# Kernel tuning notes

Hardware: AMD Instinct MI355X
Metric: run time of the kernel (lower is better)

The kernel has to match this reference:

```python
import jax, jax.numpy as jnp
import numpy as np

B0, C0, H0, W0 = 2, 64, 48, 48
BR, DI, NS, RK, K = 128, 128, 16, 4, 4
EPS = 1e-5


def _bn_relu(x, g, b):
    # eval-mode BatchNorm2d (running mean 0, var 1) followed by ReLU; x is NCHW
    return jax.nn.relu(x * (g / jnp.sqrt(1.0 + EPS))[None, :, None, None] + b[None, :, None, None])


def _c1(x, w):
    # 1x1 conv, w: (O, C, 1, 1)
    return jnp.einsum('bchw,oc->bohw', x, w[:, :, 0, 0])


def _avgpool(x, k, s, p):
    # torch AvgPool2d with count_include_pad=True -> divide by k*k
    y = jax.lax.reduce_window(x, 0.0, jax.lax.add, (1, 1, k, k), (1, 1, s, s), ((0, 0), (0, 0), (p, p), (p, p)))
    return y / float(k * k)


def _resize(x, h, w):
    # bilinear, align_corners=False (half-pixel), NCHW
    return jax.image.resize(x, (x.shape[0], x.shape[1], h, w), 'bilinear')


def _pappm(x, s0_g, s0_b, s0_w, s1_g, s1_b, s1_w, s2_g, s2_b, s2_w, s3_g, s3_b, s3_w, s4_g, s4_b, s4_w, comp_g, comp_b, comp_w, sc_g, sc_b, sc_w):
    h, w = x.shape[2], x.shape[3]
    x0 = _c1(_bn_relu(x, s0_g, s0_b), s0_w)
    y1 = _c1(_bn_relu(_avgpool(x, 3, 1, 1), s1_g, s1_b), s1_w) + x0  # stride-1 pool keeps size
    y2 = _resize(_c1(_bn_relu(_avgpool(x, 5, 2, 2), s2_g, s2_b), s2_w), h, w) + x0
    y3 = _resize(_c1(_bn_relu(_avgpool(x, 9, 4, 4), s3_g, s3_b), s3_w), h, w) + x0
    y4 = _c1(_bn_relu(x.mean((2, 3), keepdims=True), s4_g, s4_b), s4_w) + x0  # 1x1 -> broadcast
    cat = jnp.concatenate([x0, y1, y2, y3, y4], axis=1)  # (B, 5*BR, H, W)
    comp = jax.lax.conv_general_dilated(_bn_relu(cat, comp_g, comp_b), comp_w, (1, 1), ((1, 1), (1, 1)), dimension_numbers=('NCHW', 'OIHW', 'NCHW'))
    return comp + _c1(_bn_relu(x, sc_g, sc_b), sc_w)


def _ss2d(xin, in_proj_w, dw_w, dw_b, x_proj_w, dt_w, dt_b, A_logs, Ds, ln_g, ln_b, out_proj_w):
    # xin: (B, H, W, d_model)
    Bb, Hh, Ww, _ = xin.shape
    xz = xin @ in_proj_w.T                      # (B,H,W,2*DI)
    xc, z = jnp.split(xz, 2, axis=-1)
    xc = jnp.transpose(xc, (0, 3, 1, 2))        # (B,DI,H,W)
    xc = jax.lax.conv_general_dilated(xc, dw_w, (1, 1), ((1, 1), (1, 1)), dimension_numbers=('NCHW', 'OIHW', 'NCHW'), feature_group_count=DI)
    xc = jax.nn.silu(xc + dw_b[None, :, None, None])
    L = Hh * Ww
    x_hw = xc.reshape(Bb, DI, L)
    x_wh = jnp.transpose(xc, (0, 1, 3, 2)).reshape(Bb, DI, L)
    xs = jnp.stack([x_hw, x_wh, x_hw[:, :, ::-1], x_wh[:, :, ::-1]], axis=1)  # (B,K,DI,L)
    x_dbl = jnp.einsum('bkdl,kcd->bkcl', xs, x_proj_w)
    dts, Bm, Cm = jnp.split(x_dbl, [RK, RK + NS], axis=2)  # (B,K,RK,L),(B,K,NS,L),(B,K,NS,L)
    delta = jax.nn.softplus(jnp.einsum('bkrl,kdr->bkdl', dts, dt_w) + dt_b[None, :, :, None])  # (B,K,DI,L)
    A = -jnp.exp(A_logs).reshape(K, DI, NS)
    a = jnp.exp(delta[..., None] * A[None, :, :, None, :])                    # (B,K,DI,L,NS)
    bu = (delta * xs)[..., None] * jnp.transpose(Bm, (0, 1, 3, 2))[:, :, None]  # (B,K,DI,L,NS)

    def comb(e1, e2):
        a1, b1 = e1
        a2, b2 = e2
        return a2 * a1, a2 * b1 + b2

    _, hst = jax.lax.associative_scan(comb, (a, bu), axis=3)  # h_t = a_t*h_{t-1} + b_t
    y = jnp.einsum('bkdln,bknl->bkdl', hst, Cm) + xs * Ds.reshape(K, DI)[None, :, :, None]
    inv = y[:, 2:4][:, :, :, ::-1]
    y3 = jnp.transpose(y[:, 1].reshape(Bb, DI, Ww, Hh), (0, 1, 3, 2)).reshape(Bb, DI, L)
    y4 = jnp.transpose(inv[:, 1].reshape(Bb, DI, Ww, Hh), (0, 1, 3, 2)).reshape(Bb, DI, L)
    ys = jnp.transpose(y[:, 0] + inv[:, 0] + y3 + y4, (0, 2, 1)).reshape(Bb, Hh, Ww, DI)
    mu = ys.mean(-1, keepdims=True)
    var = jnp.mean((ys - mu) ** 2, -1, keepdims=True)
    yn = (ys - mu) / jnp.sqrt(var + EPS) * ln_g + ln_b
    return (yn * jax.nn.silu(z)) @ out_proj_w.T  # (B,H,W,d_model)


def setup_inputs():
    key = jax.random.key(0)
    ks = iter(jax.random.split(key, 32))
    nrm = lambda shp, s: jax.random.normal(next(ks), shp, jnp.float32) * s
    d = {}
    d['x'] = nrm((B0, C0, H0, W0), 1.0)
    for nm in ['s0', 's1', 's2', 's3', 's4']:
        d[nm + '_g'] = jnp.ones((C0,), jnp.float32)
        d[nm + '_b'] = jnp.zeros((C0,), jnp.float32)
        d[nm + '_w'] = nrm((BR, C0, 1, 1), (2.0 / C0) ** 0.5)
    d['comp_g'] = jnp.ones((5 * BR,), jnp.float32)
    d['comp_b'] = jnp.zeros((5 * BR,), jnp.float32)
    d['comp_w'] = nrm((C0, 5 * BR, 3, 3), (2.0 / (5 * BR * 9)) ** 0.5)
    d['sc_g'] = jnp.ones((C0,), jnp.float32)
    d['sc_b'] = jnp.zeros((C0,), jnp.float32)
    d['sc_w'] = nrm((C0, C0, 1, 1), (2.0 / C0) ** 0.5)
    d['in_proj_w'] = nrm((2 * DI, C0), C0 ** -0.5)
    d['dw_w'] = nrm((DI, 1, 3, 3), 0.3)
    d['dw_b'] = jnp.zeros((DI,), jnp.float32)
    d['x_proj_w'] = nrm((K, RK + 2 * NS, DI), DI ** -0.5)
    d['dt_w'] = nrm((K, DI, RK), RK ** -0.5)
    d['dt_b'] = jnp.log(jnp.expm1(jnp.asarray(0.01, jnp.float32))) * jnp.ones((K, DI), jnp.float32)
    d['A_logs'] = jnp.tile(jnp.log(jnp.arange(1, NS + 1, dtype=jnp.float32))[None], (K * DI, 1))
    d['Ds'] = jnp.ones((K * DI,), jnp.float32)
    d['ln_g'] = jnp.ones((DI,), jnp.float32)
    d['ln_b'] = jnp.zeros((DI,), jnp.float32)
    d['out_proj_w'] = nrm((C0, DI), DI ** -0.5)
    d['fc1_w'] = nrm((BR, C0, 1, 1), C0 ** -0.5)
    d['fc1_b'] = jnp.zeros((BR,), jnp.float32)
    d['fc2_w'] = nrm((C0, BR, 1, 1), BR ** -0.5)
    d['fc2_b'] = jnp.zeros((C0,), jnp.float32)
    return d


def reference(x, s0_g, s0_b, s0_w, s1_g, s1_b, s1_w, s2_g, s2_b, s2_w, s3_g, s3_b, s3_w, s4_g, s4_b, s4_w, comp_g, comp_b, comp_w, sc_g, sc_b, sc_w, in_proj_w, dw_w, dw_b, x_proj_w, dt_w, dt_b, A_logs, Ds, ln_g, ln_b, out_proj_w, fc1_w, fc1_b, fc2_w, fc2_b):
    p = _pappm(x, s0_g, s0_b, s0_w, s1_g, s1_b, s1_w, s2_g, s2_b, s2_w, s3_g, s3_b, s3_w, s4_g, s4_b, s4_w, comp_g, comp_b, comp_w, sc_g, sc_b, sc_w)
    a = _ss2d(jnp.transpose(p, (0, 2, 3, 1)), in_proj_w, dw_w, dw_b, x_proj_w, dt_w, dt_b, A_logs, Ds, ln_g, ln_b, out_proj_w)
    x1 = jnp.transpose(a, (0, 3, 1, 2))  # (B,C0,H,W)
    h1 = jax.nn.silu(_c1(x1, fc1_w) + fc1_b[None, :, None, None])
    return _c1(h1, fc2_w) + fc2_b[None, :, None, None] + x1
```

## Files before the change

### kernel.cpp

```cpp
#include <hip/hip_runtime.h>
#include <math.h>

constexpr int cB = 2, cC = 64, cH = 48, cW = 48, cL = 48 * 48;
constexpr int cBR = 128, cDI = 128, cNS = 16, cRK = 4, cK = 4;
constexpr float cEPS = 1e-5f;
constexpr int NCH = 32;
constexpr int CHL = cL / NCH;
constexpr int KTOT = 5824;

typedef unsigned short u16;
typedef unsigned int u32;
typedef short s16x8 __attribute__((ext_vector_type(8)));
typedef float f32x4 __attribute__((ext_vector_type(4)));

__device__ __forceinline__ float bnrelu(float v, float g, float b) {
    float y = v * (g * rsqrtf(1.0f + cEPS)) + b;
    return y > 0.f ? y : 0.f;
}
__device__ __forceinline__ float silu(float v) {
    return v / (1.f + expf(-v));
}
__device__ __forceinline__ u16 f2bf(float f) {
    u32 u = __float_as_uint(f);
    u = (u + 0x7fffu + ((u >> 16) & 1u)) >> 16;
    return (u16)u;
}
__device__ __forceinline__ s16x8 cvt8(const float* p) {
    s16x8 r;
#pragma unroll
    for (int i = 0; i < 8; i++) r[i] = (short)f2bf(p[i]);
    return r;
}
__device__ __forceinline__ float row_sum16(float v) {
    v += __int_as_float(__builtin_amdgcn_update_dpp(0, __float_as_int(v), 0xB1, 0xF, 0xF, true));
    v += __int_as_float(__builtin_amdgcn_update_dpp(0, __float_as_int(v), 0x4E, 0xF, 0xF, true));
    v += __int_as_float(__builtin_amdgcn_update_dpp(0, __float_as_int(v), 0x124, 0xF, 0xF, true));
    v += __int_as_float(__builtin_amdgcn_update_dpp(0, __float_as_int(v), 0x128, 0xF, 0xF, true));
    return v;
}

__global__ void __launch_bounds__(256) k_pools(const float* __restrict__ x, float* __restrict__ pool3,
                                               float* __restrict__ pool5, float* __restrict__ pool9,
                                               float* __restrict__ gmean) {
    __shared__ float sm[4];
    int blk = blockIdx.x;
    int t = threadIdx.x;
    if (blk < 1152) {
        int idx = blk * 256 + t;
        int w = idx % cW, h = (idx / cW) % cH, bc = idx / cL;
        const float* p = x + bc * cL;
        float s = 0.f;
        for (int dh = -1; dh <= 1; dh++) {
            int hh = h + dh; if (hh < 0 || hh >= cH) continue;
            for (int dw = -1; dw <= 1; dw++) {
                int ww = w + dw; if (ww < 0 || ww >= cW) continue;
                s += p[hh * cW + ww];
            }
        }
        pool3[idx] = s * (1.f / 9.f);
    } else if (blk < 1440) {
        int idx = (blk - 1152) * 256 + t;
        int w = idx % 24, h = (idx / 24) % 24, bc = idx / 576;
        const float* p = x + bc * cL;
        float s = 0.f;
        for (int kh = 0; kh < 5; kh++) {
            int hh = h * 2 - 2 + kh; if (hh < 0 || hh >= cH) continue;
            for (int kw = 0; kw < 5; kw++) {
                int ww = w * 2 - 2 + kw; if (ww < 0 || ww >= cW) continue;
                s += p[hh * cW + ww];
            }
        }
        pool5[idx] = s * (1.f / 25.f);
    } else if (blk < 1512) {
        int idx = (blk - 1440) * 256 + t;
        int w = idx % 12, h = (idx / 12) % 12, bc = idx / 144;
        const float* p = x + bc * cL;
        float s = 0.f;
        for (int kh = 0; kh < 9; kh++) {
            int hh = h * 4 - 4 + kh; if (hh < 0 || hh >= cH) continue;
            for (int kw = 0; kw < 9; kw++) {
                int ww = w * 4 - 4 + kw; if (ww < 0 || ww >= cW) continue;
                s += p[hh * cW + ww];
            }
        }
        pool9[idx] = s * (1.f / 81.f);
    } else {
        int bc = blk - 1512;
        const float* p = x + bc * cL;
        float s = 0.f;
        for (int i = t; i < cL; i += 256) s += p[i];
        for (int m = 32; m > 0; m >>= 1) s += __shfl_down(s, m);
        if ((t & 63) == 0) sm[t >> 6] = s;
        __syncthreads();
        if (t == 0) gmean[bc] = (sm[0] + sm[1] + sm[2] + sm[3]) * (1.f / cL);
    }
}

__global__ void __launch_bounds__(256) k_prep(const float* __restrict__ cw, const float* __restrict__ scw,
                                              const float* __restrict__ s0w, const float* __restrict__ s1w,
                                              const float* __restrict__ ipw, const float* __restrict__ xpw,
                                              u16* __restrict__ w8, u16* __restrict__ wcat,
                                              u16* __restrict__ ipk, u16* __restrict__ xpk) {
    int blk = blockIdx.x, t = threadIdx.x;
    if (blk < 1456) {
        int idx = blk * 256 + t;
        int o = idx / KTOT, kx = idx % KTOT;
        float v;
        if (kx < 5760) { int tap = kx / 640, ch = kx % 640; v = cw[(o * 640 + ch) * 9 + tap]; }
        else v = scw[o * 64 + (kx - 5760)];
        w8[(((size_t)(kx >> 3) * 64) + o) * 8 + (kx & 7)] = f2bf(v);
    } else if (blk < 1520) {
        int idx = (blk - 1456) * 256 + t;
        int g = idx >> 13, r = idx & 8191;
        int o = r >> 6, c = r & 63;
        float v = (g ? s1w : s0w)[r];
        int kt = c >> 5, q = (c >> 3) & 3, j = c & 7, nt = o >> 4, ln = o & 15;
        wcat[(size_t)((((g * 2 + kt) * 4 + q) * 8 + nt) * 16 + ln) * 8 + j] = f2bf(v);
    } else if (blk < 1584) {
        int idx = (blk - 1520) * 256 + t;
        int o = idx >> 6, c = idx & 63;
        int kt = c >> 5, q = (c >> 3) & 3, j = c & 7, nt = o >> 4, ln = o & 15;
        ipk[(size_t)(((kt * 4 + q) * 16 + nt) * 16 + ln) * 8 + j] = f2bf(ipw[idx]);
    } else {
        int idx = (blk - 1584) * 256 + t;
        int o = idx >> 7, d = idx & 127;
        int kt = d >> 5, q = (d >> 3) & 3, j = d & 7, nt = o >> 4, ln = o & 15;
        xpk[(size_t)(((kt * 4 + q) * 9 + nt) * 16 + ln) * 8 + j] = f2bf(xpw[idx]);
    }
}

__global__ void __launch_bounds__(128) k_c1all(const float* __restrict__ pool5, const float* __restrict__ pool9,
                                               const float* __restrict__ gm,
                                               const float* __restrict__ s2g, const float* __restrict__ s2b,
                                               const float* __restrict__ s2w,
                                               const float* __restrict__ s3g, const float* __restrict__ s3b,
                                               const float* __restrict__ s3w,
                                               const float* __restrict__ s4g, const float* __restrict__ s4b,
                                               const float* __restrict__ s4w,
                                               float* __restrict__ c2cl, float* __restrict__ c3cl,
                                               float* __restrict__ c4) {
    int pos = blockIdx.x;
    const float *in, *g, *bb, *w;
    float* outp;
    int HW, b, pp;
    if (pos < cB * 576) { b = pos / 576; pp = pos % 576; in = pool5; g = s2g; bb = s2b; w = s2w; HW = 576; outp = c2cl + ((size_t)b * 576 + pp) * 128; }
    else if (pos < cB * 576 + cB * 144) { int r = pos - cB * 576; b = r / 144; pp = r % 144; in = pool9; g = s3g; bb = s3b; w = s3w; HW = 144; outp = c3cl + ((size_t)b * 144 + pp) * 128; }
    else { b = pos - cB * 576 - cB * 144; pp = 0; in = gm; g = s4g; bb = s4b; w = s4w; HW = 1; outp = c4 + (size_t)b * 128; }
    __shared__ float v[64];
    int t = threadIdx.x;
    if (t < 64) v[t] = bnrelu(in[(b * 64 + t) * HW + pp], g[t], bb[t]);
    __syncthreads();
    float acc = 0.f;
    const float* wr = w + t * 64;
#pragma unroll 16
    for (int c = 0; c < 64; c++) acc += v[c] * wr[c];
    outp[t] = acc;
}

__global__ void __launch_bounds__(256) k_cat2(
    const float* __restrict__ x, const float* __restrict__ pool3, const float* __restrict__ c4,
    const float* __restrict__ s0g, const float* __restrict__ s0b,
    const float* __restrict__ s1g, const float* __restrict__ s1b,
    const float* __restrict__ scg, const float* __restrict__ scb,
    const float* __restrict__ cg, const float* __restrict__ cbb,
    const u16* __restrict__ wcat, const float* __restrict__ c2cl, const float* __restrict__ c3cl,
    u16* __restrict__ catbf, u16* __restrict__ xbf) {
    int blk = blockIdx.x;
    int b = blk / 144;
    int l0 = (blk % 144) * 16;
    int t = threadIdx.x;
    __shared__ float axv[16][68];
    __shared__ float ap3[16][68];
    __shared__ u16 axc[16][66];
    int pc = t >> 4, p = t & 15;
#pragma unroll
    for (int i = 0; i < 4; i++) {
        int c = i * 16 + pc;
        float xraw = x[(size_t)(b * 64 + c) * cL + l0 + p];
        float p3raw = pool3[(size_t)(b * 64 + c) * cL + l0 + p];
        axv[p][c] = bnrelu(xraw, s0g[c], s0b[c]);
        ap3[p][c] = bnrelu(p3raw, s1g[c], s1b[c]);
        axc[p][c] = f2bf(bnrelu(xraw, scg[c], scb[c]));
    }
    __syncthreads();
#pragma unroll
    for (int i = 0; i < 4; i++) {
        int idx = i * 256 + t;
        int pp = idx >> 6, cc = idx & 63;
        xbf[((size_t)b * cL + l0 + pp) * 64 + cc] = axc[pp][cc];
    }
    int wv = t >> 6, lane = t & 63, ln = lane & 15, q = lane >> 4;
    f32x4 ax[2] = {};
    f32x4 ay[2] = {};
#pragma unroll
    for (int kt = 0; kt < 2; kt++) {
        s16x8 a0 = cvt8(&axv[ln][kt * 32 + q * 8]);
        s16x8 a1 = cvt8(&ap3[ln][kt * 32 + q * 8]);
#pragma unroll
        for (int jj = 0; jj < 2; jj++) {
            int nt = wv * 2 + jj;
            s16x8 b0 = *(const s16x8*)(wcat + (size_t)((((0 * 2 + kt) * 4 + q) * 8 + nt) * 16 + ln) * 8);
            s16x8 b1 = *(const s16x8*)(wcat + (size_t)((((1 * 2 + kt) * 4 + q) * 8 + nt) * 16 + ln) * 8);
            ax[jj] = __builtin_amdgcn_mfma_f32_16x16x32_bf16(a0, b0, ax[jj], 0, 0, 0);
            ay[jj] = __builtin_amdgcn_mfma_f32_16x16x32_bf16(a1, b1, ay[jj], 0, 0, 0);
        }
    }
    int hrow = l0 / cW, w0g = l0 % cW;
    float sy2 = hrow * 0.5f - 0.25f;
    float fy2 = floorf(sy2); int iy2 = (int)fy2; float ay2 = sy2 - fy2;
    int y20 = min(max(iy2, 0), 23), y21 = min(max(iy2 + 1, 0), 23);
    float sy3 = hrow * 0.25f - 0.375f;
    float fy3 = floorf(sy3); int iy3 = (int)fy3; float ay3 = sy3 - fy3;
    int y30 = min(max(iy3, 0), 11), y31 = min(max(iy3 + 1, 0), 11);
    const float* c2b = c2cl + (size_t)b * 576 * 128;
    const float* c3b = c3cl + (size_t)b * 144 * 128;
#pragma unroll
    for (int r = 0; r < 4; r++) {
        int pp = q * 4 + r;
        int wq = w0g + pp;
        float sx2 = wq * 0.5f - 0.25f;
        float fx2 = floorf(sx2); int ix2 = (int)fx2; float ax2 = sx2 - fx2;
        int x20 = min(max(ix2, 0), 23), x21 = min(max(ix2 + 1, 0), 23);
        float sx3 = wq * 0.25f - 0.375f;
        float fx3 = floorf(sx3); int ix3 = (int)fx3; float ax3 = sx3 - fx3;
        int x30 = min(max(ix3, 0), 11), x31 = min(max(ix3 + 1, 0), 11);
#pragma unroll
        for (int jj = 0; jj < 2; jj++) {
            int ch = (wv * 2 + jj) * 16 + ln;
            float v00 = c2b[(y20 * 24 + x20) * 128 + ch], v01 = c2b[(y20 * 24 + x21) * 128 + ch];
            float v10 = c2b[(y21 * 24 + x20) * 128 + ch], v11 = c2b[(y21 * 24 + x21) * 128 + ch];
            float t0 = v00 + (v01 - v00) * ax2, t1 = v10 + (v11 - v10) * ax2;
            float u2v = t0 + (t1 - t0) * ay2;
            float w00 = c3b[(y30 * 12 + x30) * 128 + ch], w01 = c3b[(y30 * 12 + x31) * 128 + ch];
            float w10 = c3b[(y31 * 12 + x30) * 128 + ch], w11 = c3b[(y31 * 12 + x31) * 128 + ch];
            float s0_ = w00 + (w01 - w00) * ax3, s1_ = w10 + (w11 - w10) * ax3;
            float u3v = s0_ + (s1_ - s0_) * ay3;
            float x0 = ax[jj][r];
            float y1 = ay[jj][r] + x0;
            float y2 = x0 + u2v;
            float y3 = x0 + u3v;
            float y4 = x0 + c4[b * 128 + ch];
            u16* base = catbf + ((size_t)b * cL + l0 + pp) * 640;
            base[ch]       = f2bf(bnrelu(x0, cg[ch],       cbb[ch]));
            base[128 + ch] = f2bf(bnrelu(y1, cg[128 + ch], cbb[128 + ch]));
            base[256 + ch] = f2bf(bnrelu(y2, cg[256 + ch], cbb[256 + ch]));
            base[384 + ch] = f2bf(bnrelu(y3, cg[384 + ch], cbb[384 + ch]));
            base[512 + ch] = f2bf(bnrelu(y4, cg[512 + ch], cbb[512 + ch]));
        }
    }
}

__global__ void __launch_bounds__(64) k_comp(const u16* __restrict__ catbf,
                                             const u16* __restrict__ xbf,
                                             const u16* __restrict__ w8,
                                             float* __restrict__ part) {
    int blk = blockIdx.x;
    int slice = blk % 9;
    int pxt = blk / 9;
    int pix0 = pxt * 16;
    int b = pix0 / cL;
    int lane = threadIdx.x;
    int ln = lane & 15, q = lane >> 4;
    int la = (pix0 + ln) - b * cL;
    int h = la / cW, w = la % cW;
    int kh = slice / 3 - 1, kw = slice % 3 - 1;
    int hh = h + kh, ww = w + kw;
    bool ok = (hh >= 0) && (hh < cH) && (ww >= 0) && (ww < cW);
    const u16* ap = catbf + ((size_t)b * cL + hh * cW + ww) * 640 + q * 8;
    f32x4 acc[4] = {};
    int kb = slice * 640;
#pragma unroll 4
    for (int cc = 0; cc < 20; cc++) {
        s16x8 av;
        if (ok) av = *(const s16x8*)(ap + cc * 32);
        else av = s16x8{0, 0, 0, 0, 0, 0, 0, 0};
        const u16* wrow = w8 + (((size_t)((kb + cc * 32) >> 3) + q) * 64) * 8;
#pragma unroll
        for (int j = 0; j < 4; j++) {
            s16x8 bv = *(const s16x8*)(wrow + (size_t)(j * 16 + ln) * 8);
            acc[j] = __builtin_amdgcn_mfma_f32_16x16x32_bf16(av, bv, acc[j], 0, 0, 0);
        }
    }
    if (slice == 4) {
        const u16* xp = xbf + (size_t)(pix0 + ln) * 64 + q * 8;
#pragma unroll
        for (int cc = 0; cc < 2; cc++) {
            s16x8 av = *(const s16x8*)(xp + cc * 32);
            const u16* wrow = w8 + (((size_t)((5760 + cc * 32) >> 3) + q) * 64) * 8;
#pragma unroll
            for (int j = 0; j < 4; j++) {
                s16x8 bv = *(const s16x8*)(wrow + (size_t)(j * 16 + ln) * 8);
                acc[j] = __builtin_amdgcn_mfma_f32_16x16x32_bf16(av, bv, acc[j], 0, 0, 0);
            }
        }
    }
    float* pb = part + ((size_t)slice * (cB * cL) + pix0) * 64;
#pragma unroll
    for (int j = 0; j < 4; j++) {
#pragma unroll
        for (int r = 0; r < 4; r++) {
            pb[(size_t)(q * 4 + r) * 64 + j * 16 + ln] = acc[j][r];
        }
    }
}

__global__ void __launch_bounds__(256) k_ip(const float* __restrict__ part, const u16* __restrict__ ipk,
                                            float* __restrict__ xc, float* __restrict__ z) {
    int px0 = blockIdx.x * 16;
    int t = threadIdx.x;
    __shared__ float pv[16][68];
#pragma unroll
    for (int i = 0; i < 4; i++) {
        int idx = i * 256 + t;
        int p = idx >> 6, c = idx & 63;
        float s = 0.f;
#pragma unroll
        for (int sl = 0; sl < 9; sl++)
            s += part[((size_t)sl * (cB * cL) + px0 + p) * 64 + c];
        pv[p][c] = s;
    }
    __syncthreads();
    int wv = t >> 6, lane = t & 63, ln = lane & 15, q = lane >> 4;
    f32x4 acc[4] = {};
#pragma unroll
    for (int kt = 0; kt < 2; kt++) {
        s16x8 a = cvt8(&pv[ln][kt * 32 + q * 8]);
#pragma unroll
        for (int jn = 0; jn < 4; jn++) {
            int nt = wv * 4 + jn;
            s16x8 bfr = *(const s16x8*)(ipk + (size_t)(((kt * 4 + q) * 16 + nt) * 16 + ln) * 8);
            acc[jn] = __builtin_amdgcn_mfma_f32_16x16x32_bf16(a, bfr, acc[jn], 0, 0, 0);
        }
    }
#pragma unroll
    for (int jn = 0; jn < 4; jn++) {
        int o = (wv * 4 + jn) * 16 + ln;
#pragma unroll
        for (int r = 0; r < 4; r++) {
            int p = q * 4 + r;
            if (o < 128) xc[((size_t)px0 + p) * 128 + o] = acc[jn][r];
            else         z[((size_t)px0 + p) * 128 + (o - 128)] = acc[jn][r];
        }
    }
}

__global__ void k_dw(const float* __restrict__ xc, const float* __restrict__ dww,
                     const float* __restrict__ dwb, float* __restrict__ xca) {
    int idx = blockIdx.x * 256 + threadIdx.x;
    if (idx >= cB * cL * cDI) return;
    int d = idx & 127;
    int rest = idx >> 7;
    int l = rest % cL, b = rest / cL;
    int h = l / cW, w = l % cW;
    const float* base = xc + (size_t)b * cL * 128 + d;
    float acc = dwb[d];
    const float* kw = dww + d * 9;
    for (int i = 0; i < 3; i++) {
        int hh = h + i - 1; if (hh < 0 || hh >= cH) continue;
        for (int j = 0; j < 3; j++) {
            int ww = w + j - 1; if (ww < 0 || ww >= cW) continue;
            acc += base[(size_t)(hh * cW + ww) * 128] * kw[i * 3 + j];
        }
    }
    xca[idx] = silu(acc);
}

__global__ void __launch_bounds__(256) k_xdbl4(const float* __restrict__ xca, const u16* __restrict__ xpk,
                                               const float* __restrict__ dtw, const float* __restrict__ dtb,
                                               float* __restrict__ bc, float* __restrict__ delta) {
    int blk = blockIdx.x;
    int b = blk / 144;
    int l0 = (blk % 144) * 16;
    int t = threadIdx.x;
    __shared__ float av[16][132];
    __shared__ float Dt[16][148];
#pragma unroll
    for (int i = 0; i < 8; i++) {
        int id = i * 256 + t;
        int d = id & 127, p = id >> 7;
        av[p][d] = xca[((size_t)b * cL + l0 + p) * 128 + d];
    }
    __syncthreads();
    int wv = t >> 6, lane = t & 63, ln = lane & 15, q = lane >> 4;
    int nmax = (wv == 0) ? 3 : 2;
    f32x4 acc[3] = {};
#pragma unroll
    for (int kt = 0; kt < 4; kt++) {
        s16x8 a = cvt8(&av[ln][kt * 32 + q * 8]);
        for (int i = 0; i < nmax; i++) {
            int nt = (i == 2) ? 8 : wv + i * 4;
            s16x8 bfr = *(const s16x8*)(xpk + (size_t)(((kt * 4 + q) * 9 + nt) * 16 + ln) * 8);
            acc[i] = __builtin_amdgcn_mfma_f32_16x16x32_bf16(a, bfr, acc[i], 0, 0, 0);
        }
    }
    for (int i = 0; i < nmax; i++) {
        int nt = (i == 2) ? 8 : wv + i * 4;
#pragma unroll
        for (int r = 0; r < 4; r++)
            Dt[q * 4 + r][nt * 16 + ln] = acc[i][r];
    }
    __syncthreads();
#pragma unroll
    for (int i = 0; i < 8; i++) {
        int id = i * 256 + t;
        int cc = id & 31, kk = (id >> 5) & 3, p = id >> 7;
        bc[((size_t)(b * 4 + kk) * cL + l0 + p) * 32 + cc] = Dt[p][kk * 36 + 4 + cc];
    }
    for (int i = 0; i < 32; i++) {
        int id = i * 256 + t;
        int d = id & 127, kk = (id >> 7) & 3, p = id >> 9;
        const float* wd = dtw + (size_t)(kk * 128 + d) * 4;
        float pre = dtb[kk * 128 + d] + wd[0] * Dt[p][kk * 36] + wd[1] * Dt[p][kk * 36 + 1]
                  + wd[2] * Dt[p][kk * 36 + 2] + wd[3] * Dt[p][kk * 36 + 3];
        float dl = pre > 20.f ? pre : log1pf(expf(pre));
        delta[((size_t)(b * 4 + kk) * cL + l0 + p) * 128 + d] = dl;
    }
}

__device__ __forceinline__ int xs_index(int k, int l) {
    int lp = (k & 2) ? (cL - 1 - l) : l;
    if (k & 1) { int w = lp / cH, h = lp % cH; return h * cW + w; }
    return lp;
}

__global__ void __launch_bounds__(256) k_scan1(const float* __restrict__ delta, const float* __restrict__ xca,
                                               const float* __restrict__ bc, const float* __restrict__ Alogs,
                                               float* __restrict__ Pend, float* __restrict__ hend) {
    int blk = blockIdx.x;
    int c = blk & 31;
    if (c == NCH - 1) return;
    int g = blk >> 5;
    int dgq = g & 7, bk = g >> 3;
    int k = bk & 3, b = bk >> 2;
    int t = threadIdx.x;
    int n = t & 15;
    int d = dgq * 16 + (t >> 4);
    float A = -expf(Alogs[(k * 128 + d) * 16 + n]);
    const float* dp = delta + (size_t)bk * cL * 128 + d;
    const float* xp = xca + (size_t)b * cL * 128 + d;
    const float* bp = bc + (size_t)bk * cL * 32 + n;
    int off = xs_index(k, c * CHL);
    int step = (k == 0) ? 1 : (k == 1) ? cW : (k == 2) ? -1 : -cW;
    float P = 1.f, h = 0.f;
#pragma unroll 4
    for (int i = 0; i < CHL; i++) {
        float dl = dp[(size_t)off * 128];
        float a = expf(dl * A);
        h = a * h + dl * xp[(size_t)off * 128] * bp[(size_t)off * 32];
        P *= a;
        off += step;
        if (off >= cL) off -= (cL - 1);
        else if (off < 0) off += (cL - 1);
    }
    Pend[(size_t)blk * 256 + t] = P;
    hend[(size_t)blk * 256 + t] = h;
}

__global__ void __launch_bounds__(256) k_scan2(const float* __restrict__ Pend, float* __restrict__ hend) {
    int id = blockIdx.x * 256 + threadIdx.x;
    int t = id & 255;
    int g = id >> 8;
    float h = 0.f;
    for (int c = 0; c < NCH; c++) {
        size_t idx = ((size_t)g * NCH + c) * 256 + t;
        float tmp = hend[idx];
        float Pv = Pend[idx];
        hend[idx] = h;
        h = Pv * h + tmp;
    }
}

__global__ void __launch_bounds__(256) k_scan3(const float* __restrict__ delta, const float* __restrict__ xca,
                                               const float* __restrict__ bc, const float* __restrict__ Alogs,
                                               const float* __restrict__ Dsv, const float* __restrict__ hinb,
                                               float* __restrict__ y) {
    int blk = blockIdx.x;
    int c = blk & 31;
    int g = blk >> 5;
    int dgq = g & 7, bk = g >> 3;
    int k = bk & 3, b = bk >> 2;
    int t = threadIdx.x;
    int n = t & 15;
    int d = dgq * 16 + (t >> 4);
    float A = -expf(Alogs[(k * 128 + d) * 16 + n]);
    float Dsd = Dsv[k * 128 + d];
    const float* dp = delta + (size_t)bk * cL * 128 + d;
    const float* xp = xca + (size_t)b * cL * 128 + d;
    const float* bp = bc + (size_t)bk * cL * 32 + n;
    const float* cp = bc + (size_t)bk * cL * 32 + 16 + n;
    float* yb = y + (size_t)bk * cL * 128 + d;
    int off = xs_index(k, c * CHL);
    int step = (k == 0) ? 1 : (k == 1) ? cW : (k == 2) ? -1 : -cW;
    float h = hinb[(size_t)blk * 256 + t];
#pragma unroll 2
    for (int i = 0; i < CHL; i++) {
        float dl = dp[(size_t)off * 128];
        float xv = xp[(size_t)off * 128];
        float a = expf(dl * A);
        h = a * h + dl * xv * bp[(size_t)off * 32];
        float contrib = row_sum16(h * cp[(size_t)off * 32]);
        if (n == 0) yb[(size_t)off * 128] = contrib + xv * Dsd;
        off += step;
        if (off >= cL) off -= (cL - 1);
        else if (off < 0) off += (cL - 1);
    }
}

__global__ void __launch_bounds__(256) k_tail(const float* __restrict__ y, const float* __restrict__ z,
                                              const float* __restrict__ lng, const float* __restrict__ lnb,
                                              const float* __restrict__ opw,
                                              const float* __restrict__ f1w, const float* __restrict__ f1b,
                                              const float* __restrict__ f2w, const float* __restrict__ f2b,
                                              float* __restrict__ out) {
    int blk = blockIdx.x;
    int b = blk / 144;
    int l0 = (blk % 144) * 16;
    int t = threadIdx.x;
    __shared__ float v[16][132];
    __shared__ float x1s[16][68];
    __shared__ float h1s[16][132];
    __shared__ float mus[16], rss[16];
    const float* yb = y + (size_t)b * 4 * cL * 128;
#pragma unroll
    for (int i = 0; i < 8; i++) {
        int id = i * 256 + t;
        int d = id & 127, p = id >> 7;
        size_t base = (size_t)(l0 + p) * 128 + d;
        v[p][d] = yb[base] + yb[(size_t)cL * 128 + base] + yb[(size_t)2 * cL * 128 + base] + yb[(size_t)3 * cL * 128 + base];
    }
    __syncthreads();
    {
        int p = t >> 4, c8 = (t & 15) * 8;
        float s = 0.f;
#pragma unroll
        for (int j = 0; j < 8; j++) s += v[p][c8 + j];
        s = row_sum16(s);
        float mu = s * (1.f / 128.f);
        float s2 = 0.f;
#pragma unroll
        for (int j = 0; j < 8; j++) { float dv = v[p][c8 + j] - mu; s2 += dv * dv; }
        s2 = row_sum16(s2);
        if ((t & 15) == 0) { mus[p] = mu; rss[p] = rsqrtf(s2 * (1.f / 128.f) + cEPS); }
    }
    __syncthreads();
#pragma unroll
    for (int i = 0; i < 8; i++) {
        int id = i * 256 + t;
        int d = id & 127, p = id >> 7;
        float zz = z[((size_t)b * cL + l0 + p) * 128 + d];
        v[p][d] = ((v[p][d] - mus[p]) * rss[p] * lng[d] + lnb[d]) * silu(zz);
    }
    __syncthreads();
#pragma unroll
    for (int i = 0; i < 4; i++) {
        int id = i * 256 + t;
        int p = id & 15, o = id >> 4;
        const float* wr = opw + o * 128;
        float acc = 0.f;
#pragma unroll 16
        for (int d2 = 0; d2 < 128; d2++) acc += v[p][d2] * wr[d2];
        x1s[p][o] = acc;
    }
    __syncthreads();
#pragma unroll
    for (int i = 0; i < 8; i++) {
        int id = i * 256 + t;
        int p = id & 15, j = id >> 4;
        const float* wr = f1w + j * 64;
        float acc = f1b[j];
#pragma unroll 16
        for (int c = 0; c < 64; c++) acc += x1s[p][c] * wr[c];
        h1s[p][j] = silu(acc);
    }
    __syncthreads();
#pragma unroll
    for (int i = 0; i < 4; i++) {
        int id = i * 256 + t;
        int p = id & 15, o = id >> 4;
        const float* wr = f2w + o * 128;
        float acc = f2b[o];
#pragma unroll 16
        for (int j = 0; j < 128; j++) acc += h1s[p][j] * wr[j];
        out[((size_t)b * 64 + o) * cL + l0 + p] = acc + x1s[p][o];
    }
}

extern "C" void kernel_launch(void* const* d_in, const int* in_sizes, int n_in,
                              void* d_out, int out_size, void* d_ws, size_t ws_size,
                              hipStream_t stream) {
    (void)in_sizes; (void)n_in; (void)out_size; (void)ws_size;
    const float* x    = (const float*)d_in[0];
    const float* s0g  = (const float*)d_in[1];
    const float* s0b  = (const float*)d_in[2];
    const float* s0w  = (const float*)d_in[3];
    const float* s1g  = (const float*)d_in[4];
    const float* s1b  = (const float*)d_in[5];
    const float* s1w  = (const float*)d_in[6];
    const float* s2g  = (const float*)d_in[7];
    const float* s2b  = (const float*)d_in[8];
    const float* s2w  = (const float*)d_in[9];
    const float* s3g  = (const float*)d_in[10];
    const float* s3b  = (const float*)d_in[11];
    const float* s3w  = (const float*)d_in[12];
    const float* s4g  = (const float*)d_in[13];
    const float* s4b  = (const float*)d_in[14];
    const float* s4w  = (const float*)d_in[15];
    const float* cg   = (const float*)d_in[16];
    const float* cbb  = (const float*)d_in[17];
    const float* cw   = (const float*)d_in[18];
    const float* scg  = (const float*)d_in[19];
    const float* scb  = (const float*)d_in[20];
    const float* scw  = (const float*)d_in[21];
    const float* ipw  = (const float*)d_in[22];
    const float* dww  = (const float*)d_in[23];
    const float* dwb  = (const float*)d_in[24];
    const float* xpw  = (const float*)d_in[25];
    const float* dtw  = (const float*)d_in[26];
    const float* dtb  = (const float*)d_in[27];
    const float* Alog = (const float*)d_in[28];
    const float* Dsv  = (const float*)d_in[29];
    const float* lng  = (const float*)d_in[30];
    const float* lnb  = (const float*)d_in[31];
    const float* opw  = (const float*)d_in[32];
    const float* f1w  = (const float*)d_in[33];
    const float* f1b  = (const float*)d_in[34];
    const float* f2w  = (const float*)d_in[35];
    const float* f2b  = (const float*)d_in[36];
    float* out = (float*)d_out;

    float* ws = (float*)d_ws;
    size_t off = 0;
    float* pool3  = ws + off; off += 294912;
    float* pool5  = ws + off; off += 73728;
    float* pool9  = ws + off; off += 18432;
    float* gmean  = ws + off; off += 128;
    float* c2cl   = ws + off; off += 147456;
    float* c3cl   = ws + off; off += 36864;
    float* c4     = ws + off; off += 256;
    u16*   catbf  = (u16*)(ws + off); off += 1474560;
    u16*   xbf    = (u16*)(ws + off); off += 147456;
    u16*   w8     = (u16*)(ws + off); off += 186368;
    u16*   wcat   = (u16*)(ws + off); off += 8192;
    u16*   ipk    = (u16*)(ws + off); off += 8192;
    float* xc     = ws + off; off += 589824;
    u16*   xpk    = (u16*)(ws + off); off += 9216;
    float* xca    = ws + off; off += 589824;
    float* zbuf   = ws + off; off += 589824;
    float* bcbuf  = ws + off; off += 589824;
    float* Pend   = ws + off; off += 524288;
    float* ybuf   = ws + off; off += 2359296;
    off += 294912;
    float* delta  = ws + 0;
    float* hend   = xc;
    float* part   = ybuf;

    k_pools<<<1640, 256, 0, stream>>>(x, pool3, pool5, pool9, gmean);
    k_prep<<<1656, 256, 0, stream>>>(cw, scw, s0w, s1w, ipw, xpw, w8, wcat, ipk, xpk);
    k_c1all<<<cB * 576 + cB * 144 + cB, 128, 0, stream>>>(pool5, pool9, gmean, s2g, s2b, s2w,
                                                          s3g, s3b, s3w, s4g, s4b, s4w, c2cl, c3cl, c4);
    k_cat2<<<cB * 144, 256, 0, stream>>>(x, pool3, c4, s0g, s0b, s1g, s1b, scg, scb, cg, cbb,
                                         wcat, c2cl, c3cl, catbf, xbf);
    k_comp<<<(cB * cL / 16) * 9, 64, 0, stream>>>(catbf, xbf, w8, part);
    k_ip<<<cB * cL / 16, 256, 0, stream>>>(part, ipk, xc, zbuf);
    k_dw<<<(cB * cL * 128 + 255) / 256, 256, 0, stream>>>(xc, dww, dwb, xca);
    k_xdbl4<<<cB * 144, 256, 0, stream>>>(xca, xpk, dtw, dtb, bcbuf, delta);
    k_scan1<<<64 * NCH, 256, 0, stream>>>(delta, xca, bcbuf, Alog, Pend, hend);
    k_scan2<<<64, 256, 0, stream>>>(Pend, hend);
    k_scan3<<<64 * NCH, 256, 0, stream>>>(delta, xca, bcbuf, Alog, Dsv, hend, ybuf);
    k_tail<<<cB * 144, 256, 0, stream>>>(ybuf, zbuf, lng, lnb, opw, f1w, f1b, f2w, f2b, out);
}
```

Measured before the change: 304.3 us.

## Double scan chunk count, interleave B/C for float2 loads, merge pools and prep

```diff
diff --git a/kernel.cpp b/kernel.cpp
--- a/kernel.cpp
+++ b/kernel.cpp
@@ -4,7 +4,7 @@
 constexpr int cB = 2, cC = 64, cH = 48, cW = 48, cL = 48 * 48;
 constexpr int cBR = 128, cDI = 128, cNS = 16, cRK = 4, cK = 4;
 constexpr float cEPS = 1e-5f;
-constexpr int NCH = 32;
+constexpr int NCH = 64;
 constexpr int CHL = cL / NCH;
 constexpr int KTOT = 5824;
 
@@ -39,9 +39,14 @@
     return v;
 }
 
-__global__ void __launch_bounds__(256) k_pools(const float* __restrict__ x, float* __restrict__ pool3,
-                                               float* __restrict__ pool5, float* __restrict__ pool9,
-                                               float* __restrict__ gmean) {
+__global__ void __launch_bounds__(256) k_setup(
+    const float* __restrict__ x, float* __restrict__ pool3, float* __restrict__ pool5,
+    float* __restrict__ pool9, float* __restrict__ gmean,
+    const float* __restrict__ cw, const float* __restrict__ scw,
+    const float* __restrict__ s0w, const float* __restrict__ s1w,
+    const float* __restrict__ ipw, const float* __restrict__ xpw,
+    u16* __restrict__ w8, u16* __restrict__ wcat,
+    u16* __restrict__ ipk, u16* __restrict__ xpk) {
     __shared__ float sm[4];
     int blk = blockIdx.x;
     int t = threadIdx.x;
@@ -84,7 +89,7 @@
             }
         }
         pool9[idx] = s * (1.f / 81.f);
-    } else {
+    } else if (blk < 1640) {
         int bc = blk - 1512;
         const float* p = x + bc * cL;
         float s = 0.f;
@@ -93,39 +98,33 @@
         if ((t & 63) == 0) sm[t >> 6] = s;
         __syncthreads();
         if (t == 0) gmean[bc] = (sm[0] + sm[1] + sm[2] + sm[3]) * (1.f / cL);
-    }
-}
-
-__global__ void __launch_bounds__(256) k_prep(const float* __restrict__ cw, const float* __restrict__ scw,
-                                              const float* __restrict__ s0w, const float* __restrict__ s1w,
-                                              const float* __restrict__ ipw, const float* __restrict__ xpw,
-                                              u16* __restrict__ w8, u16* __restrict__ wcat,
-                                              u16* __restrict__ ipk, u16* __restrict__ xpk) {
-    int blk = blockIdx.x, t = threadIdx.x;
-    if (blk < 1456) {
-        int idx = blk * 256 + t;
-        int o = idx / KTOT, kx = idx % KTOT;
-        float v;
-        if (kx < 5760) { int tap = kx / 640, ch = kx % 640; v = cw[(o * 640 + ch) * 9 + tap]; }
-        else v = scw[o * 64 + (kx - 5760)];
-        w8[(((size_t)(kx >> 3) * 64) + o) * 8 + (kx & 7)] = f2bf(v);
-    } else if (blk < 1520) {
-        int idx = (blk - 1456) * 256 + t;
-        int g = idx >> 13, r = idx & 8191;
-        int o = r >> 6, c = r & 63;
-        float v = (g ? s1w : s0w)[r];
-        int kt = c >> 5, q = (c >> 3) & 3, j = c & 7, nt = o >> 4, ln = o & 15;
-        wcat[(size_t)((((g * 2 + kt) * 4 + q) * 8 + nt) * 16 + ln) * 8 + j] = f2bf(v);
-    } else if (blk < 1584) {
-        int idx = (blk - 1520) * 256 + t;
-        int o = idx >> 6, c = idx & 63;
-        int kt = c >> 5, q = (c >> 3) & 3, j = c & 7, nt = o >> 4, ln = o & 15;
-        ipk[(size_t)(((kt * 4 + q) * 16 + nt) * 16 + ln) * 8 + j] = f2bf(ipw[idx]);
     } else {
-        int idx = (blk - 1584) * 256 + t;
-        int o = idx >> 7, d = idx & 127;
-        int kt = d >> 5, q = (d >> 3) & 3, j = d & 7, nt = o >> 4, ln = o & 15;
-        xpk[(size_t)(((kt * 4 + q) * 9 + nt) * 16 + ln) * 8 + j] = f2bf(xpw[idx]);
+        int pblk = blk - 1640;
+        if (pblk < 1456) {
+            int idx = pblk * 256 + t;
+            int o = idx / KTOT, kx = idx % KTOT;
+            float v;
+            if (kx < 5760) { int tap = kx / 640, ch = kx % 640; v = cw[(o * 640 + ch) * 9 + tap]; }
+            else v = scw[o * 64 + (kx - 5760)];
+            w8[(((size_t)(kx >> 3) * 64) + o) * 8 + (kx & 7)] = f2bf(v);
+        } else if (pblk < 1520) {
+            int idx = (pblk - 1456) * 256 + t;
+            int g = idx >> 13, r = idx & 8191;
+            int o = r >> 6, c = r & 63;
+            float v = (g ? s1w : s0w)[r];
+            int kt = c >> 5, q = (c >> 3) & 3, j = c & 7, nt = o >> 4, ln = o & 15;
+            wcat[(size_t)((((g * 2 + kt) * 4 + q) * 8 + nt) * 16 + ln) * 8 + j] = f2bf(v);
+        } else if (pblk < 1584) {
+            int idx = (pblk - 1520) * 256 + t;
+            int o = idx >> 6, c = idx & 63;
+            int kt = c >> 5, q = (c >> 3) & 3, j = c & 7, nt = o >> 4, ln = o & 15;
+            ipk[(size_t)(((kt * 4 + q) * 16 + nt) * 16 + ln) * 8 + j] = f2bf(ipw[idx]);
+        } else {
+            int idx = (pblk - 1584) * 256 + t;
+            int o = idx >> 7, d = idx & 127;
+            int kt = d >> 5, q = (d >> 3) & 3, j = d & 7, nt = o >> 4, ln = o & 15;
+            xpk[(size_t)(((kt * 4 + q) * 9 + nt) * 16 + ln) * 8 + j] = f2bf(xpw[idx]);
+        }
     }
 }
 
@@ -404,7 +403,8 @@
     for (int i = 0; i < 8; i++) {
         int id = i * 256 + t;
         int cc = id & 31, kk = (id >> 5) & 3, p = id >> 7;
-        bc[((size_t)(b * 4 + kk) * cL + l0 + p) * 32 + cc] = Dt[p][kk * 36 + 4 + cc];
+        int slot = (cc < 16) ? (cc * 2) : ((cc - 16) * 2 + 1);
+        bc[((size_t)(b * 4 + kk) * cL + l0 + p) * 32 + slot] = Dt[p][kk * 36 + 4 + cc];
     }
     for (int i = 0; i < 32; i++) {
         int id = i * 256 + t;
@@ -427,9 +427,9 @@
                                                const float* __restrict__ bc, const float* __restrict__ Alogs,
                                                float* __restrict__ Pend, float* __restrict__ hend) {
     int blk = blockIdx.x;
-    int c = blk & 31;
+    int c = blk & 63;
     if (c == NCH - 1) return;
-    int g = blk >> 5;
+    int g = blk >> 6;
     int dgq = g & 7, bk = g >> 3;
     int k = bk & 3, b = bk >> 2;
     int t = threadIdx.x;
@@ -438,15 +438,16 @@
     float A = -expf(Alogs[(k * 128 + d) * 16 + n]);
     const float* dp = delta + (size_t)bk * cL * 128 + d;
     const float* xp = xca + (size_t)b * cL * 128 + d;
-    const float* bp = bc + (size_t)bk * cL * 32 + n;
+    const float* bp = bc + (size_t)bk * cL * 32 + n * 2;
     int off = xs_index(k, c * CHL);
     int step = (k == 0) ? 1 : (k == 1) ? cW : (k == 2) ? -1 : -cW;
     float P = 1.f, h = 0.f;
 #pragma unroll 4
     for (int i = 0; i < CHL; i++) {
         float dl = dp[(size_t)off * 128];
+        float2 bcv = *(const float2*)(bp + (size_t)off * 32);
         float a = expf(dl * A);
-        h = a * h + dl * xp[(size_t)off * 128] * bp[(size_t)off * 32];
+        h = a * h + dl * xp[(size_t)off * 128] * bcv.x;
         P *= a;
         off += step;
         if (off >= cL) off -= (cL - 1);
@@ -475,8 +476,8 @@
                                                const float* __restrict__ Dsv, const float* __restrict__ hinb,
                                                float* __restrict__ y) {
     int blk = blockIdx.x;
-    int c = blk & 31;
-    int g = blk >> 5;
+    int c = blk & 63;
+    int g = blk >> 6;
     int dgq = g & 7, bk = g >> 3;
     int k = bk & 3, b = bk >> 2;
     int t = threadIdx.x;
@@ -486,8 +487,7 @@
     float Dsd = Dsv[k * 128 + d];
     const float* dp = delta + (size_t)bk * cL * 128 + d;
     const float* xp = xca + (size_t)b * cL * 128 + d;
-    const float* bp = bc + (size_t)bk * cL * 32 + n;
-    const float* cp = bc + (size_t)bk * cL * 32 + 16 + n;
+    const float* bp = bc + (size_t)bk * cL * 32 + n * 2;
     float* yb = y + (size_t)bk * cL * 128 + d;
     int off = xs_index(k, c * CHL);
     int step = (k == 0) ? 1 : (k == 1) ? cW : (k == 2) ? -1 : -cW;
@@ -496,9 +496,10 @@
     for (int i = 0; i < CHL; i++) {
         float dl = dp[(size_t)off * 128];
         float xv = xp[(size_t)off * 128];
+        float2 bcv = *(const float2*)(bp + (size_t)off * 32);
         float a = expf(dl * A);
-        h = a * h + dl * xv * bp[(size_t)off * 32];
-        float contrib = row_sum16(h * cp[(size_t)off * 32]);
+        h = a * h + dl * xv * bcv.x;
+        float contrib = row_sum16(h * bcv.y);
         if (n == 0) yb[(size_t)off * 128] = contrib + xv * Dsd;
         off += step;
         if (off >= cL) off -= (cL - 1);
@@ -647,15 +648,15 @@
     float* xca    = ws + off; off += 589824;
     float* zbuf   = ws + off; off += 589824;
     float* bcbuf  = ws + off; off += 589824;
-    float* Pend   = ws + off; off += 524288;
+    float* Pend   = ws + off; off += 1048576;
+    float* hend   = ws + off; off += 1048576;
     float* ybuf   = ws + off; off += 2359296;
     off += 294912;
     float* delta  = ws + 0;
-    float* hend   = xc;
     float* part   = ybuf;
 
-    k_pools<<<1640, 256, 0, stream>>>(x, pool3, pool5, pool9, gmean);
-    k_prep<<<1656, 256, 0, stream>>>(cw, scw, s0w, s1w, ipw, xpw, w8, wcat, ipk, xpk);
+    k_setup<<<3296, 256, 0, stream>>>(x, pool3, pool5, pool9, gmean,
+                                      cw, scw, s0w, s1w, ipw, xpw, w8, wcat, ipk, xpk);
     k_c1all<<<cB * 576 + cB * 144 + cB, 128, 0, stream>>>(pool5, pool9, gmean, s2g, s2b, s2w,
                                                           s3g, s3b, s3w, s4g, s4b, s4w, c2cl, c3cl, c4);
     k_cat2<<<cB * 144, 256, 0, stream>>>(x, pool3, c4, s0g, s0b, s1g, s1b, scg, scb, cg, cbb,
```

Measured after the change: 308.9 us. Within noise of the previous version (+1.5%).
